# Optimization experiments

Hardware: AMD Instinct MI355X
Metric: run time of the kernel (lower is better)

The kernel has to match this reference:

```python
import jax, jax.numpy as jnp
import numpy as np

B, N = 512, 256

def setup_inputs() -> dict:
    key = jax.random.key(0)
    k1, k2 = jax.random.split(key)
    D1 = jax.random.normal(k1, (B, N, N), dtype=jnp.float32)
    D2 = jax.random.normal(k2, (B, N, N), dtype=jnp.float32)
    types1 = jnp.zeros((B, N), dtype=jnp.int32)
    types2 = jnp.zeros((B, N), dtype=jnp.int32)
    return {"D1": D1, "D2": D2, "types1": types1, "types2": types2}


def reference(D1, D2, types1, types2):
    # Hungarian cost: cost[b, i, j] = |mean_k D1[b, k, i] - mean_k D2[b, k, j]|.
    # For an absolute-difference cost between two scalar profiles, the optimal
    # linear assignment (what scipy's linear_sum_assignment returns inside the
    # original tf.py_function) matches sorted values to sorted values; with a
    # point-type constraint, it matches sorted values within each type group.
    # We therefore compute the exact optimal permutation via a lexicographic
    # sort on (type, mean-distance) for each side, which is fully vectorized
    # and avoids the host-side CPU loop of the original layer.
    a = jnp.mean(D1, axis=1)  # [B, N] column means of D1
    b = jnp.mean(D2, axis=1)  # [B, N]

    def optimal_perm(a_row, b_row, t1, t2):
        # sort primarily by type, secondarily by value (lexsort: last key primary)
        order1 = jnp.lexsort((a_row, t1))  # [N] atom indices of D1 in sorted order
        order2 = jnp.lexsort((b_row, t2))  # [N] target positions in sorted order
        # atom order1[k] is placed at position order2[k]
        return jnp.zeros_like(order1).at[order2].set(order1)  # perm[j] = source atom for slot j

    perm = jax.vmap(optimal_perm)(a, b, types1, types2)  # [B, N]

    # Symmetric reorder of rows and columns of D1 by perm.
    D1_rows = jnp.take_along_axis(D1, perm[:, :, None], axis=1)          # [B, N, N]
    D1_reordered = jnp.take_along_axis(D1_rows, perm[:, None, :], axis=2)  # [B, N, N]
    types1_reordered = jnp.take_along_axis(types1, perm, axis=1)         # [B, N]

    # The original layer applies tf.stop_gradient to both outputs.
    D1_reordered = jax.lax.stop_gradient(D1_reordered)
    types1_reordered = jax.lax.stop_gradient(types1_reordered)
    return D1_reordered, types1_reordered
```

## Files before the change

### kernel.cpp

```cpp
#include <hip/hip_runtime.h>

#define BATCH 512
#define NN 256

typedef __attribute__((ext_vector_type(4))) float f32x4;

__device__ __forceinline__ float4 f4add(float4 x, float4 y) {
  return make_float4(x.x + y.x, x.y + y.y, x.z + y.z, x.w + y.w);
}

__device__ __forceinline__ void dma_row16(const float* g, float* l) {
  __builtin_amdgcn_global_load_lds(
      (const __attribute__((address_space(1))) void*)g,
      (__attribute__((address_space(3))) void*)l, 16, 0, 0);
}

__global__ __launch_bounds__(512, 4) void fused_hungarian_kernel(
    const float* __restrict__ D1, const float* __restrict__ D2,
    const int* __restrict__ t1, const int* __restrict__ t2,
    float* __restrict__ out, float* __restrict__ types_out) {
  const int b = blockIdx.x;
  const int tid = threadIdx.x;
  const int lane = tid & 63;
  const int wv = tid >> 6;

  __shared__ __align__(16) char smem[73728];
  float* const stagef = (float*)smem;
  float* const va = (float*)smem;
  float* const vb = (float*)(smem + 1024);
  int* const ta = (int*)(smem + 2048);
  int* const tb = (int*)(smem + 3072);
  int* const ord1 = (int*)(smem + 4096);
  int* const ord2 = (int*)(smem + 5120);
  int* const plds = (int*)(smem + 6144);
  float4* const rows = (float4*)(smem + 8192);
  float* const partialf = (float*)(smem + 65536);

  {
    const int mat = wv >> 2;
    const int s2 = wv & 3;
    const int h = s2 >> 1;
    const int tq = s2 & 1;
    const float* __restrict__ src = (mat ? D2 : D1) + (size_t)b * (NN * NN);
    const float* cb = src + (size_t)(h * 128 + 4 * tq) * NN;
    float* const wstage = stagef + wv * 2048;

#pragma unroll
    for (int mk = 0; mk < 8; ++mk) {
      const int m = mk >> 2, k = mk & 3;
      dma_row16(cb + (size_t)(8 * m + k) * NN + 4 * lane,
                wstage + ((m & 1) * 4 + k) * 256);
    }

    float4 r0, r1, r2, r3;
#pragma unroll
    for (int m = 0; m < 16; ++m) {
      if (m == 15) asm volatile("s_waitcnt vmcnt(0)" ::: "memory");
      else         asm volatile("s_waitcnt vmcnt(4)" ::: "memory");
      const float* sp = wstage + (m & 1) * 1024 + 4 * lane;
      const float4 v0 = *(const float4*)(sp + 0);
      const float4 v1 = *(const float4*)(sp + 256);
      const float4 v2 = *(const float4*)(sp + 512);
      const float4 v3 = *(const float4*)(sp + 768);
      asm volatile("s_waitcnt lgkmcnt(0)" ::: "memory");
      if (m + 2 < 16) {
#pragma unroll
        for (int k = 0; k < 4; ++k)
          dma_row16(cb + (size_t)(8 * (m + 2) + k) * NN + 4 * lane,
                    wstage + ((m & 1) * 4 + k) * 256);
      }
      if (m == 0) { r0 = v0; r1 = v1; r2 = v2; r3 = v3; }
      else {
        r0 = f4add(r0, v0); r1 = f4add(r1, v1);
        r2 = f4add(r2, v2); r3 = f4add(r3, v3);
      }
    }
    const float4 part = f4add(f4add(r0, r1), f4add(r2, r3));
    *(float4*)(partialf + (mat * 4 + s2) * 256 + 4 * lane) = part;
  }
  __syncthreads();

  {
    const int mat = tid >> 8;
    const int c = tid & 255;
    const float p0 = partialf[(mat * 4 + 0) * 256 + c];
    const float p1 = partialf[(mat * 4 + 1) * 256 + c];
    const float p2 = partialf[(mat * 4 + 2) * 256 + c];
    const float p3 = partialf[(mat * 4 + 3) * 256 + c];
    const float mean = ((p0 + p1) + (p2 + p3)) * (1.0f / 256.0f);
    if (mat == 0) { va[c] = mean; ta[c] = t1[b * NN + c]; }
    else          { vb[c] = mean; tb[c] = t2[b * NN + c]; }
  }
  __syncthreads();

  {
    const int side = tid >> 8;
    const int c = tid & 255;
    const float* __restrict__ vv = side ? vb : va;
    const int* __restrict__ tt = side ? tb : ta;
    const float vi = vv[c];
    const int ti = tt[c];
    int r = 0;
#pragma unroll 4
    for (int j = 0; j < NN; ++j) {
      const int tj = tt[j];
      const float vj = vv[j];
      const bool less =
          (tj < ti) || (tj == ti && (vj < vi || (vj == vi && j < c)));
      r += less ? 1 : 0;
    }
    if (side == 0) ord1[r] = c;
    else           ord2[r] = c;
  }
  __syncthreads();
  if (tid < NN) plds[ord2[tid]] = ord1[tid];
  __syncthreads();
  if (tid < NN) types_out[b * NN + tid] = (float)ta[plds[tid]];

  {
    const int j0 = 4 * lane;
    const int pj0 = plds[j0 + 0];
    const int pj1 = plds[j0 + 1];
    const int pj2 = plds[j0 + 2];
    const int pj3 = plds[j0 + 3];
    const float* __restrict__ Db = D1 + (size_t)b * (NN * NN);
    float* __restrict__ outb = out + (size_t)b * (NN * NN);
    const float* const rowf = (const float*)(rows + wv * 64);

    float4 vA = *(const float4*)(Db + (size_t)plds[wv] * NN + j0);
    float4 vB = *(const float4*)(Db + (size_t)plds[8 + wv] * NN + j0);
#pragma unroll 4
    for (int iter = 0; iter < 32; ++iter) {
      rows[wv * 64 + lane] = vA;
      vA = vB;
      if (iter + 2 < 32)
        vB = *(const float4*)(Db + (size_t)plds[(iter + 2) * 8 + wv] * NN + j0);
      float4 o;
      o.x = rowf[pj0];
      o.y = rowf[pj1];
      o.z = rowf[pj2];
      o.w = rowf[pj3];
      __builtin_nontemporal_store(
          *(const f32x4*)&o,
          (f32x4*)(outb + (size_t)(iter * 8 + wv) * NN + j0));
    }
  }
}

extern "C" void kernel_launch(void* const* d_in, const int* in_sizes, int n_in,
                              void* d_out, int out_size, void* d_ws, size_t ws_size,
                              hipStream_t stream) {
  const float* D1 = (const float*)d_in[0];
  const float* D2 = (const float*)d_in[1];
  const int* t1 = (const int*)d_in[2];
  const int* t2 = (const int*)d_in[3];

  float* out = (float*)d_out;
  float* types_out = out + (size_t)BATCH * NN * NN;

  fused_hungarian_kernel<<<BATCH, 512, 0, stream>>>(D1, D2, t1, t2, out,
                                                    types_out);
}
```

Measured before the change: 343.2 us.

## Process batch pairs per block, overlapping second mean-load with first gather

Each block now handles two batch items. While the first item's permuted output is written, the column-sum loads for the second item are interleaved. The first 128 rows of D1 from the first item are kept in a 128KB LDS buffer, so half the gather reads come from LDS instead of being re-read from global memory. Blocks drop from 512 to 256, LDS use rises to about 151KB, and global_load_lds DMA is replaced by plain vector loads, which cuts occupancy and parallelism.

```diff
diff --git a/kernel.cpp b/kernel.cpp
--- a/kernel.cpp
+++ b/kernel.cpp
@@ -2,6 +2,7 @@
 
 #define BATCH 512
 #define NN 256
+#define MSZ (NN * NN)
 
 typedef __attribute__((ext_vector_type(4))) float f32x4;
 
@@ -9,65 +10,71 @@
   return make_float4(x.x + y.x, x.y + y.y, x.z + y.z, x.w + y.w);
 }
 
-__device__ __forceinline__ void dma_row16(const float* g, float* l) {
-  __builtin_amdgcn_global_load_lds(
-      (const __attribute__((address_space(1))) void*)g,
-      (__attribute__((address_space(3))) void*)l, 16, 0, 0);
-}
-
-__global__ __launch_bounds__(512, 4) void fused_hungarian_kernel(
+__device__ __forceinline__ void rank_side(const float* __restrict__ vv,
+                                          const int* __restrict__ tt, int c,
+                                          int* __restrict__ ordX) {
+  const float vi = vv[c];
+  const int ti = tt[c];
+  int r = 0;
+#pragma unroll 4
+  for (int j = 0; j < NN; ++j) {
+    const int tj = tt[j];
+    const float vj = vv[j];
+    const bool less =
+        (tj < ti) || (tj == ti && (vj < vi || (vj == vi && j < c)));
+    r += less ? 1 : 0;
+  }
+  ordX[r] = c;
+}
+
+__global__ __launch_bounds__(512, 2) void fused_pair_kernel(
     const float* __restrict__ D1, const float* __restrict__ D2,
     const int* __restrict__ t1, const int* __restrict__ t2,
     float* __restrict__ out, float* __restrict__ types_out) {
-  const int b = blockIdx.x;
+  const int b0 = 2 * blockIdx.x;
+  const int b1 = b0 + 1;
   const int tid = threadIdx.x;
   const int lane = tid & 63;
   const int wv = tid >> 6;
 
-  __shared__ __align__(16) char smem[73728];
-  float* const stagef = (float*)smem;
-  float* const va = (float*)smem;
-  float* const vb = (float*)(smem + 1024);
-  int* const ta = (int*)(smem + 2048);
-  int* const tb = (int*)(smem + 3072);
-  int* const ord1 = (int*)(smem + 4096);
-  int* const ord2 = (int*)(smem + 5120);
-  int* const plds = (int*)(smem + 6144);
-  float4* const rows = (float4*)(smem + 8192);
-  float* const partialf = (float*)(smem + 65536);
-
-  {
-    const int mat = wv >> 2;
-    const int s2 = wv & 3;
-    const int h = s2 >> 1;
-    const int tq = s2 & 1;
-    const float* __restrict__ src = (mat ? D2 : D1) + (size_t)b * (NN * NN);
-    const float* cb = src + (size_t)(h * 128 + 4 * tq) * NN;
-    float* const wstage = stagef + wv * 2048;
-
-#pragma unroll
-    for (int mk = 0; mk < 8; ++mk) {
-      const int m = mk >> 2, k = mk & 3;
-      dma_row16(cb + (size_t)(8 * m + k) * NN + 4 * lane,
-                wstage + ((m & 1) * 4 + k) * 256);
-    }
+  __shared__ __align__(16) char smem[154624];
+  float* const d1rows = (float*)smem;
+  float* const partialf = (float*)(smem + 131072);
+  float* const va = (float*)(smem + 139264);
+  float* const vb = (float*)(smem + 140288);
+  int* const ta = (int*)(smem + 141312);
+  int* const tb = (int*)(smem + 142336);
+  int* const ord1 = (int*)(smem + 143360);
+  int* const ord2 = (int*)(smem + 144384);
+  int* const plds = (int*)(smem + 145408);
+  float4* const rows = (float4*)(smem + 146432);
+
+  const int mat = wv >> 2;
+  const int s2 = wv & 3;
+  const int h = s2 >> 1;
+  const int tq = s2 & 1;
+  const int j0 = 4 * lane;
+
+  {
+    const float* __restrict__ src = (mat ? D2 : D1) + (size_t)b0 * MSZ;
+    const float* cb = src + (size_t)(h * 128 + 4 * tq) * NN + j0;
+    const bool persist = (wv < 2);
+    float* const prow = d1rows + (size_t)(4 * tq) * NN + j0;
 
     float4 r0, r1, r2, r3;
 #pragma unroll
     for (int m = 0; m < 16; ++m) {
-      if (m == 15) asm volatile("s_waitcnt vmcnt(0)" ::: "memory");
-      else         asm volatile("s_waitcnt vmcnt(4)" ::: "memory");
-      const float* sp = wstage + (m & 1) * 1024 + 4 * lane;
-      const float4 v0 = *(const float4*)(sp + 0);
-      const float4 v1 = *(const float4*)(sp + 256);
-      const float4 v2 = *(const float4*)(sp + 512);
-      const float4 v3 = *(const float4*)(sp + 768);
-      asm volatile("s_waitcnt lgkmcnt(0)" ::: "memory");
-      if (m + 2 < 16) {
-#pragma unroll
-        for (int k = 0; k < 4; ++k)
-          dma_row16(cb + (size_t)(8 * (m + 2) + k) * NN + 4 * lane,
-                    wstage + ((m & 1) * 4 + k) * 256);
+      const float* p = cb + (size_t)(8 * m) * NN;
+      const float4 v0 = *(const float4*)(p + (size_t)0 * NN);
+      const float4 v1 = *(const float4*)(p + (size_t)1 * NN);
+      const float4 v2 = *(const float4*)(p + (size_t)2 * NN);
+      const float4 v3 = *(const float4*)(p + (size_t)3 * NN);
+      if (persist) {
+        float* q = prow + (size_t)(8 * m) * NN;
+        *(float4*)(q + (size_t)0 * NN) = v0;
+        *(float4*)(q + (size_t)1 * NN) = v1;
+        *(float4*)(q + (size_t)2 * NN) = v2;
+        *(float4*)(q + (size_t)3 * NN) = v3;
       }
       if (m == 0) { r0 = v0; r1 = v1; r2 = v2; r3 = v3; }
       else {
@@ -76,73 +83,127 @@
       }
     }
     const float4 part = f4add(f4add(r0, r1), f4add(r2, r3));
-    *(float4*)(partialf + (mat * 4 + s2) * 256 + 4 * lane) = part;
-  }
-  __syncthreads();
-
-  {
-    const int mat = tid >> 8;
-    const int c = tid & 255;
-    const float p0 = partialf[(mat * 4 + 0) * 256 + c];
-    const float p1 = partialf[(mat * 4 + 1) * 256 + c];
-    const float p2 = partialf[(mat * 4 + 2) * 256 + c];
-    const float p3 = partialf[(mat * 4 + 3) * 256 + c];
+    *(float4*)(partialf + (size_t)(mat * 4 + s2) * NN + j0) = part;
+  }
+  __syncthreads();
+
+  {
+    const int cm = tid >> 8, c = tid & 255;
+    const float p0 = partialf[(cm * 4 + 0) * NN + c];
+    const float p1 = partialf[(cm * 4 + 1) * NN + c];
+    const float p2 = partialf[(cm * 4 + 2) * NN + c];
+    const float p3 = partialf[(cm * 4 + 3) * NN + c];
     const float mean = ((p0 + p1) + (p2 + p3)) * (1.0f / 256.0f);
-    if (mat == 0) { va[c] = mean; ta[c] = t1[b * NN + c]; }
-    else          { vb[c] = mean; tb[c] = t2[b * NN + c]; }
-  }
-  __syncthreads();
-
-  {
-    const int side = tid >> 8;
-    const int c = tid & 255;
-    const float* __restrict__ vv = side ? vb : va;
-    const int* __restrict__ tt = side ? tb : ta;
-    const float vi = vv[c];
-    const int ti = tt[c];
-    int r = 0;
-#pragma unroll 4
-    for (int j = 0; j < NN; ++j) {
-      const int tj = tt[j];
-      const float vj = vv[j];
-      const bool less =
-          (tj < ti) || (tj == ti && (vj < vi || (vj == vi && j < c)));
-      r += less ? 1 : 0;
-    }
-    if (side == 0) ord1[r] = c;
-    else           ord2[r] = c;
+    if (cm == 0) { va[c] = mean; ta[c] = t1[b0 * NN + c]; }
+    else         { vb[c] = mean; tb[c] = t2[b0 * NN + c]; }
+  }
+  __syncthreads();
+  {
+    const int side = tid >> 8, c = tid & 255;
+    rank_side(side ? vb : va, side ? tb : ta, c, side ? ord2 : ord1);
   }
   __syncthreads();
   if (tid < NN) plds[ord2[tid]] = ord1[tid];
   __syncthreads();
-  if (tid < NN) types_out[b * NN + tid] = (float)ta[plds[tid]];
-
-  {
-    const int j0 = 4 * lane;
+  if (tid < NN) types_out[b0 * NN + tid] = (float)ta[plds[tid]];
+
+  {
     const int pj0 = plds[j0 + 0];
     const int pj1 = plds[j0 + 1];
     const int pj2 = plds[j0 + 2];
     const int pj3 = plds[j0 + 3];
-    const float* __restrict__ Db = D1 + (size_t)b * (NN * NN);
-    float* __restrict__ outb = out + (size_t)b * (NN * NN);
-    const float* const rowf = (const float*)(rows + wv * 64);
-
-    float4 vA = *(const float4*)(Db + (size_t)plds[wv] * NN + j0);
-    float4 vB = *(const float4*)(Db + (size_t)plds[8 + wv] * NN + j0);
+    const float* __restrict__ srcA = (mat ? D2 : D1) + (size_t)b1 * MSZ;
+    const float* cbA = srcA + (size_t)(h * 128 + 4 * tq) * NN + j0;
+    const float* __restrict__ Db0 = D1 + (size_t)b0 * MSZ;
+    float* __restrict__ outb0 = out + (size_t)b0 * MSZ;
+    float4* const roww = rows + wv * 64;
+    const float* const rowf = (const float*)roww;
+
+    auto c_iter = [&](int t) {
+      const int i = t * 8 + wv;
+      const int pi = plds[i];
+      float4 o;
+      if (pi < 128) {
+        const float* base = d1rows + (size_t)pi * NN;
+        o.x = base[pj0]; o.y = base[pj1]; o.z = base[pj2]; o.w = base[pj3];
+      } else {
+        const float4 v = *(const float4*)(Db0 + (size_t)pi * NN + j0);
+        roww[lane] = v;
+        o.x = rowf[pj0]; o.y = rowf[pj1]; o.z = rowf[pj2]; o.w = rowf[pj3];
+      }
+      __builtin_nontemporal_store(*(const f32x4*)&o,
+                                  (f32x4*)(outb0 + (size_t)i * NN + j0));
+    };
+
+    float4 q0 = *(const float4*)(cbA + (size_t)0 * NN);
+    float4 q1 = *(const float4*)(cbA + (size_t)1 * NN);
+    float4 q2 = *(const float4*)(cbA + (size_t)2 * NN);
+    float4 q3 = *(const float4*)(cbA + (size_t)3 * NN);
+    float4 r0, r1, r2, r3;
+#pragma unroll
+    for (int m = 0; m < 16; ++m) {
+      c_iter(2 * m);
+      if (m == 0) { r0 = q0; r1 = q1; r2 = q2; r3 = q3; }
+      else {
+        r0 = f4add(r0, q0); r1 = f4add(r1, q1);
+        r2 = f4add(r2, q2); r3 = f4add(r3, q3);
+      }
+      if (m < 15) {
+        const float* p = cbA + (size_t)(8 * (m + 1)) * NN;
+        q0 = *(const float4*)(p + (size_t)0 * NN);
+        q1 = *(const float4*)(p + (size_t)1 * NN);
+        q2 = *(const float4*)(p + (size_t)2 * NN);
+        q3 = *(const float4*)(p + (size_t)3 * NN);
+      }
+      c_iter(2 * m + 1);
+    }
+    const float4 part = f4add(f4add(r0, r1), f4add(r2, r3));
+    *(float4*)(partialf + (size_t)(mat * 4 + s2) * NN + j0) = part;
+  }
+  __syncthreads();
+
+  {
+    const int cm = tid >> 8, c = tid & 255;
+    const float p0 = partialf[(cm * 4 + 0) * NN + c];
+    const float p1 = partialf[(cm * 4 + 1) * NN + c];
+    const float p2 = partialf[(cm * 4 + 2) * NN + c];
+    const float p3 = partialf[(cm * 4 + 3) * NN + c];
+    const float mean = ((p0 + p1) + (p2 + p3)) * (1.0f / 256.0f);
+    if (cm == 0) { va[c] = mean; ta[c] = t1[b1 * NN + c]; }
+    else         { vb[c] = mean; tb[c] = t2[b1 * NN + c]; }
+  }
+  __syncthreads();
+  {
+    const int side = tid >> 8, c = tid & 255;
+    rank_side(side ? vb : va, side ? tb : ta, c, side ? ord2 : ord1);
+  }
+  __syncthreads();
+  if (tid < NN) plds[ord2[tid]] = ord1[tid];
+  __syncthreads();
+  if (tid < NN) types_out[b1 * NN + tid] = (float)ta[plds[tid]];
+
+  {
+    const int pj0 = plds[j0 + 0];
+    const int pj1 = plds[j0 + 1];
+    const int pj2 = plds[j0 + 2];
+    const int pj3 = plds[j0 + 3];
+    const float* __restrict__ Db1 = D1 + (size_t)b1 * MSZ;
+    float* __restrict__ outb1 = out + (size_t)b1 * MSZ;
+    float4* const roww = rows + wv * 64;
+    const float* const rowf = (const float*)roww;
+
+    float4 vA = *(const float4*)(Db1 + (size_t)plds[wv] * NN + j0);
+    float4 vB = *(const float4*)(Db1 + (size_t)plds[8 + wv] * NN + j0);
 #pragma unroll 4
-    for (int iter = 0; iter < 32; ++iter) {
-      rows[wv * 64 + lane] = vA;
+    for (int it = 0; it < 32; ++it) {
+      roww[lane] = vA;
       vA = vB;
-      if (iter + 2 < 32)
-        vB = *(const float4*)(Db + (size_t)plds[(iter + 2) * 8 + wv] * NN + j0);
+      if (it + 2 < 32)
+        vB = *(const float4*)(Db1 + (size_t)plds[(it + 2) * 8 + wv] * NN + j0);
       float4 o;
-      o.x = rowf[pj0];
-      o.y = rowf[pj1];
-      o.z = rowf[pj2];
-      o.w = rowf[pj3];
-      __builtin_nontemporal_store(
-          *(const f32x4*)&o,
-          (f32x4*)(outb + (size_t)(iter * 8 + wv) * NN + j0));
+      o.x = rowf[pj0]; o.y = rowf[pj1]; o.z = rowf[pj2]; o.w = rowf[pj3];
+      __builtin_nontemporal_store(*(const f32x4*)&o,
+                                  (f32x4*)(outb1 + (size_t)(it * 8 + wv) * NN + j0));
     }
   }
 }
@@ -158,6 +219,6 @@
   float* out = (float*)d_out;
   float* types_out = out + (size_t)BATCH * NN * NN;
 
-  fused_hungarian_kernel<<<BATCH, 512, 0, stream>>>(D1, D2, t1, t2, out,
-                                                    types_out);
-}
+  fused_pair_kernel<<<BATCH / 2, 512, 0, stream>>>(D1, D2, t1, t2, out,
+                                                   types_out);
+}
```

Result: slower. 375.6 us (+9.4%).
